# Performance work log

Measured on AMD Instinct MI355X. Metric: run time of the kernel, lower is better.

The kernel has to match this reference:

```python
import jax, jax.numpy as jnp
import numpy as np

SEQ, IN_DIM, OUT_DIM = 8192, 1024, 1024

def setup_inputs() -> dict:
    key = jax.random.key(0)
    k1, k2, k3, k4 = jax.random.split(key, 4)
    inputs = jax.random.normal(k1, (SEQ, IN_DIM), dtype=jnp.float32)
    # torch.nn.Linear stores weight as [out_dim, in_dim]; y = x @ W.T
    w_query = jax.random.normal(k2, (OUT_DIM, IN_DIM), dtype=jnp.float32) * (1.0 / np.sqrt(IN_DIM))
    w_key = jax.random.normal(k3, (OUT_DIM, IN_DIM), dtype=jnp.float32) * (1.0 / np.sqrt(IN_DIM))
    w_value = jax.random.normal(k4, (OUT_DIM, IN_DIM), dtype=jnp.float32) * (1.0 / np.sqrt(IN_DIM))
    return {"inputs": inputs, "w_query": w_query, "w_key": w_key, "w_value": w_value}

def reference(inputs, w_query, w_key, w_value):
    # QKV projections: [S, D_out]
    q = inputs @ w_query.T
    k = inputs @ w_key.T
    v = inputs @ w_value.T
    scale = 1.0 / jnp.sqrt(jnp.asarray(k.shape[-1], dtype=q.dtype))
    scores = (q @ k.T) * scale  # [S, S]
    # causal mask: lower-triangular kept, upper set to -inf
    s = scores.shape[0]
    causal = jnp.tril(jnp.ones((s, s), dtype=bool))
    scores = jnp.where(causal, scores, -jnp.inf)
    attn = jax.nn.softmax(scores, axis=-1)
    return attn @ v
```

## Files before the change

kernel.cpp:

```cpp
#include <hip/hip_runtime.h>
#include <stdint.h>
#include <stddef.h>


#define SEQ   8192
#define DIM   1024

typedef __bf16 bf16x8 __attribute__((ext_vector_type(8)));
typedef float  f32x4  __attribute__((ext_vector_type(4)));

#define MFMA16(a, b, c) __builtin_amdgcn_mfma_f32_16x16x32_bf16((a), (b), (c), 0, 0, 0)

__device__ __forceinline__ uint16_t f2bf(float f) {
  uint32_t u = __builtin_bit_cast(uint32_t, f);
  return (uint16_t)((u + 0x7fffu + ((u >> 16) & 1u)) >> 16);
}
__device__ __forceinline__ float bf2f(uint16_t h) {
  uint32_t u = ((uint32_t)h) << 16;
  return __builtin_bit_cast(float, u);
}

typedef const __attribute__((address_space(1))) uint32_t* gas_t;
typedef __attribute__((address_space(3))) uint32_t* las_t;
__device__ __forceinline__ void async16(const void* g, void* l) {
  __builtin_amdgcn_global_load_lds((gas_t)g, (las_t)l, 16, 0, 0);
}

__global__ __launch_bounds__(256) void cast_all(const float* __restrict__ x,
                                                const float* __restrict__ wq,
                                                const float* __restrict__ wk,
                                                const float* __restrict__ wv,
                                                uint16_t* __restrict__ xb,
                                                uint16_t* __restrict__ wcat) {
  int b = blockIdx.x;
  const float* src;
  uint16_t* dst;
  int i;
  if (b < 8192) {
    src = x; dst = xb; i = (b * 256 + threadIdx.x) * 4;
  } else {
    int wb = b - 8192;
    int sel = wb >> 10;
    src = sel == 0 ? wq : (sel == 1 ? wk : wv);
    dst = wcat + sel * 1048576;
    i = ((wb & 1023) * 256 + threadIdx.x) * 4;
  }
  float4 v = *(const float4*)(src + i);
  ushort4 o;
  o.x = f2bf(v.x); o.y = f2bf(v.y); o.z = f2bf(v.z); o.w = f2bf(v.w);
  *(ushort4*)(dst + i) = o;
}

__global__ __launch_bounds__(256) void qkv_gemm(const uint16_t* __restrict__ A,
                                                const uint16_t* __restrict__ B,
                                                uint16_t* __restrict__ Qblk,
                                                uint16_t* __restrict__ Kblk,
                                                uint16_t* __restrict__ Vblk) {
  __shared__ __align__(16) uint16_t Sh[16384];
  uint16_t* As = Sh;
  uint16_t* Bs = Sh + 8192;
  const int t    = threadIdx.x;
  const int w    = t >> 6;
  const int lane = t & 63;
  const int lm   = lane & 15;
  const int qd   = lane >> 4;
  const int wrow = (w >> 1) * 64;
  const int wcol = (w & 1) * 64;
  const int rowbase = blockIdx.y * 128;
  const int colbase = blockIdx.x * 128;

  const int lrow = lane >> 3;
  const int lgrp = (lane & 7) ^ (lrow & 7);

  f32x4 acc[4][4] = {};

  for (int kb = 0; kb < DIM; kb += 64) {
    __syncthreads();
#pragma unroll
    for (int rep = 0; rep < 4; ++rep) {
      int r0 = rep * 32 + w * 8;
      async16(A + (size_t)(rowbase + r0 + lrow) * DIM + kb + lgrp * 8, As + r0 * 64);
      async16(B + (size_t)(colbase + r0 + lrow) * DIM + kb + lgrp * 8, Bs + r0 * 64);
    }
    __syncthreads();
#pragma unroll
    for (int kc = 0; kc < 2; ++kc) {
      bf16x8 af[4], bfr[4];
#pragma unroll
      for (int mt = 0; mt < 4; ++mt) {
        int r = wrow + mt * 16 + lm;
        af[mt] = *(const bf16x8*)(As + r * 64 + (((kc * 4 + qd) ^ (lm & 7)) * 8));
      }
#pragma unroll
      for (int nt = 0; nt < 4; ++nt) {
        int r = wcol + nt * 16 + lm;
        bfr[nt] = *(const bf16x8*)(Bs + r * 64 + (((kc * 4 + qd) ^ (lm & 7)) * 8));
      }
#pragma unroll
      for (int mt = 0; mt < 4; ++mt)
#pragma unroll
        for (int nt = 0; nt < 4; ++nt)
          acc[mt][nt] = MFMA16(af[mt], bfr[nt], acc[mt][nt]);
    }
  }

  __syncthreads();
#pragma unroll
  for (int mt = 0; mt < 4; ++mt)
#pragma unroll
    for (int nt = 0; nt < 4; ++nt)
#pragma unroll
      for (int r = 0; r < 4; ++r) {
        int ml = wrow + mt * 16 + qd * 4 + r;
        int nl = wcol + nt * 16 + lm;
        uint16_t v = f2bf(acc[mt][nt][r]);
        int off;
        if (colbase < 2048) {
          off = ((ml >> 4) * 4 + (nl >> 5)) * 512 + ((nl >> 3) & 3) * 128 +
                (ml & 15) * 8 + (nl & 7);
        } else {
          off = ((nl >> 4) * 4 + (ml >> 5)) * 512 + ((ml >> 3) & 3) * 128 +
                (nl & 15) * 8 + (ml & 7);
        }
        Sh[off] = v;
      }
  __syncthreads();

  {
    uint16_t* dst = colbase < 1024 ? Qblk : (colbase < 2048 ? Kblk : Vblk);
    const int cb = colbase & 1023;
#pragma unroll
    for (int i = 0; i < 8; ++i) {
      int ch  = i * 256 + t;
      int tf  = ch >> 6;
      int idx = ch & 63;
      size_t gbase;
      if (colbase < 2048)
        gbase = ((size_t)((rowbase >> 4) + (tf >> 2)) * 32 + (cb >> 5) + (tf & 3)) * 512;
      else
        gbase = ((size_t)((cb >> 4) + (tf >> 2)) * 256 + (rowbase >> 5) + (tf & 3)) * 512;
      *(float4*)(dst + gbase + idx * 8) = *(const float4*)(Sh + tf * 512 + idx * 8);
    }
  }
}

__global__ __launch_bounds__(1024) void attn_kernel(const uint16_t* __restrict__ Qblk,
                                                    const uint16_t* __restrict__ Kblk,
                                                    const uint16_t* __restrict__ Vblk,
                                                    uint16_t* __restrict__ P0,
                                                    uint16_t* __restrict__ P1,
                                                    float* __restrict__ Mm,
                                                    float* __restrict__ Ll) {
  __shared__ __align__(16) uint16_t Qs[32768];
  __shared__ __align__(16) uint16_t Pb[8192];
  __shared__ float stats[32][16];
  __shared__ float mrow[32];

  const int t    = threadIdx.x;
  const int w    = t >> 6;
  const int lane = t & 63;
  const int lm   = lane & 15;
  const int qd   = lane >> 4;
  const int slot = blockIdx.x >> 3;
  const int p    = (blockIdx.x & 7) * 16 + (slot >> 1);
  const int par  = slot & 1;
  const float c1 = 0.045084220027780106f;

#pragma unroll 1
  for (int half = 0; half < 2; ++half) {
    const int tt   = half ? 255 - p : p;
    const int row0 = tt * 32;
    const int jn   = (tt >> 3) + 1;

    __syncthreads();
#pragma unroll
    for (int i = 0; i < 4; ++i)
      async16(Qblk + ((size_t)(tt * 64 + w * 4 + i)) * 512 + lane * 8,
              Qs + (w * 4 + i) * 512);

    bf16x8 kr[4];
    {
      const uint16_t* kbp0 = Kblk + ((size_t)(par * 16 + w) * 32) * 512 + lane * 8;
#pragma unroll
      for (int c = 0; c < 4; ++c)
        kr[c] = *(const bf16x8*)(kbp0 + (size_t)c * 512);
    }
    __syncthreads();

    float m_run[2][4], l_run[2][4];
#pragma unroll
    for (int mt = 0; mt < 2; ++mt)
#pragma unroll
      for (int r = 0; r < 4; ++r) { m_run[mt][r] = -1e30f; l_run[mt][r] = 0.0f; }
    f32x4 o_acc[2][4] = {};

#pragma unroll 1
    for (int jg = par; jg < jn; jg += 2) {
      const uint16_t* kbp = Kblk + ((size_t)(jg * 16 + w) * 32) * 512 + lane * 8;
      const uint16_t* vbp = Vblk + ((size_t)(w * 4) * 256 + jg * 8) * 512 + lane * 8;
      const uint16_t* qsp = Qs + lane * 8;

      f32x4 sacc[2] = {};
#pragma unroll
      for (int kb = 0; kb < 32; ++kb) {
        bf16x8 q0 = *(const bf16x8*)(qsp + kb * 512);
        bf16x8 q1 = *(const bf16x8*)(qsp + (32 + kb) * 512);
        bf16x8 kcur = kr[kb & 3];
        if (kb < 28)
          kr[kb & 3] = *(const bf16x8*)(kbp + (size_t)(kb + 4) * 512);
        sacc[0] = MFMA16(q0, kcur, sacc[0]);
        sacc[1] = MFMA16(q1, kcur, sacc[1]);
      }

      if (jg == jn - 1) {
#pragma unroll
        for (int mt = 0; mt < 2; ++mt)
#pragma unroll
          for (int r = 0; r < 4; ++r) {
            int col = jg * 256 + w * 16 + lm;
            int row = row0 + mt * 16 + qd * 4 + r;
            if (col > row) sacc[mt][r] = -1e30f;
          }
      }

#pragma unroll
      for (int mt = 0; mt < 2; ++mt)
#pragma unroll
        for (int r = 0; r < 4; ++r) {
          float v = sacc[mt][r];
          v = fmaxf(v, __shfl_xor(v, 1));
          v = fmaxf(v, __shfl_xor(v, 2));
          v = fmaxf(v, __shfl_xor(v, 4));
          v = fmaxf(v, __shfl_xor(v, 8));
          if (lm == 0) stats[mt * 16 + qd * 4 + r][w] = v;
        }
      __syncthreads();

      bf16x8 vr0[4], vr1[4];
#pragma unroll
      for (int dt = 0; dt < 4; ++dt)
        vr0[dt] = *(const bf16x8*)(vbp + ((size_t)dt * 256 + 0) * 512);

      float alpha[2][4], psum[2][4];
#pragma unroll
      for (int mt = 0; mt < 2; ++mt)
#pragma unroll
        for (int r = 0; r < 4; ++r) {
          int rl = mt * 16 + qd * 4 + r;
          float4 g0 = *(const float4*)&stats[rl][0];
          float4 g1 = *(const float4*)&stats[rl][4];
          float4 g2 = *(const float4*)&stats[rl][8];
          float4 g3 = *(const float4*)&stats[rl][12];
          float gm = fmaxf(
              fmaxf(fmaxf(fmaxf(g0.x, g0.y), fmaxf(g0.z, g0.w)),
                    fmaxf(fmaxf(g1.x, g1.y), fmaxf(g1.z, g1.w))),
              fmaxf(fmaxf(fmaxf(g2.x, g2.y), fmaxf(g2.z, g2.w)),
                    fmaxf(fmaxf(g3.x, g3.y), fmaxf(g3.z, g3.w))));
          float mn = fmaxf(m_run[mt][r], gm);
          alpha[mt][r] = exp2f((m_run[mt][r] - mn) * c1);
          m_run[mt][r] = mn;
          psum[mt][r] = 0.0f;
        }
#pragma unroll
      for (int mt = 0; mt < 2; ++mt)
#pragma unroll
        for (int r = 0; r < 4; ++r) {
          float pv = exp2f((sacc[mt][r] - m_run[mt][r]) * c1);
          psum[mt][r] += pv;
          Pb[((mt * 8 + (w >> 1)) * 64 + ((w & 1) * 2 + (lm >> 3)) * 16 +
              qd * 4 + r) * 8 + (lm & 7)] = f2bf(pv);
        }

#pragma unroll
      for (int dt = 0; dt < 4; ++dt)
        vr1[dt] = *(const bf16x8*)(vbp + ((size_t)dt * 256 + 1) * 512);

#pragma unroll
      for (int mt = 0; mt < 2; ++mt)
#pragma unroll
        for (int r = 0; r < 4; ++r) {
          float s2 = psum[mt][r];
          s2 += __shfl_xor(s2, 1);
          s2 += __shfl_xor(s2, 2);
          s2 += __shfl_xor(s2, 4);
          s2 += __shfl_xor(s2, 8);
          l_run[mt][r] = l_run[mt][r] * alpha[mt][r] + s2;
        }
      __syncthreads();

      {
        const uint16_t* kbpn = Kblk + ((size_t)((jg + 2) * 16 + w) * 32) * 512 + lane * 8;
#pragma unroll
        for (int c = 0; c < 4; ++c)
          kr[c] = *(const bf16x8*)(kbpn + (size_t)c * 512);
      }

#pragma unroll
      for (int mt = 0; mt < 2; ++mt)
#pragma unroll
        for (int dt = 0; dt < 4; ++dt)
#pragma unroll
          for (int r = 0; r < 4; ++r)
            o_acc[mt][dt][r] *= alpha[mt][r];

#pragma unroll
      for (int kc = 0; kc < 8; ++kc) {
        bf16x8 pf0 = *(const bf16x8*)(Pb + (kc * 64 + lane) * 8);
        bf16x8 pf1 = *(const bf16x8*)(Pb + ((8 + kc) * 64 + lane) * 8);
#pragma unroll
        for (int dt = 0; dt < 4; ++dt) {
          bf16x8 vf = (kc & 1) ? vr1[dt] : vr0[dt];
          o_acc[0][dt] = MFMA16(pf0, vf, o_acc[0][dt]);
          o_acc[1][dt] = MFMA16(pf1, vf, o_acc[1][dt]);
        }
        if (kc < 6) {
#pragma unroll
          for (int dt = 0; dt < 4; ++dt) {
            if (kc & 1)
              vr1[dt] = *(const bf16x8*)(vbp + ((size_t)dt * 256 + kc + 2) * 512);
            else
              vr0[dt] = *(const bf16x8*)(vbp + ((size_t)dt * 256 + kc + 2) * 512);
          }
        }
      }
    }

    if (lm == 0) {
#pragma unroll
      for (int mt = 0; mt < 2; ++mt)
#pragma unroll
        for (int r = 0; r < 4; ++r) {
          int rl = mt * 16 + qd * 4 + r;
          stats[rl][w] = l_run[mt][r];
          if (w == 0) mrow[rl] = m_run[mt][r];
        }
    }
    __syncthreads();
    if (t < 32) {
      float4 a0 = *(const float4*)&stats[t][0];
      float4 a1 = *(const float4*)&stats[t][4];
      float4 a2 = *(const float4*)&stats[t][8];
      float4 a3 = *(const float4*)&stats[t][12];
      Mm[par * SEQ + row0 + t] = mrow[t];
      Ll[par * SEQ + row0 + t] = (a0.x + a0.y + a0.z + a0.w) +
                                 (a1.x + a1.y + a1.z + a1.w) +
                                 (a2.x + a2.y + a2.z + a2.w) +
                                 (a3.x + a3.y + a3.z + a3.w);
    }
    uint16_t* Pp = par ? P1 : P0;
#pragma unroll
    for (int mt = 0; mt < 2; ++mt)
#pragma unroll
      for (int dt = 0; dt < 4; ++dt)
#pragma unroll
        for (int r = 0; r < 4; ++r) {
          int row = row0 + mt * 16 + qd * 4 + r;
          int d   = w * 64 + dt * 16 + lm;
          Pp[(size_t)row * DIM + d] = f2bf(o_acc[mt][dt][r]);
        }
  }
}

__global__ __launch_bounds__(256) void merge_kernel(const uint16_t* __restrict__ P0,
                                                    const uint16_t* __restrict__ P1,
                                                    const float* __restrict__ Mm,
                                                    const float* __restrict__ Ll,
                                                    float* __restrict__ out) {
  const int row = blockIdx.x;
  const int d0  = threadIdx.x * 4;
  const float c1 = 0.045084220027780106f;
  float m0 = Mm[row], m1 = Mm[SEQ + row];
  float l0 = Ll[row], l1 = Ll[SEQ + row];
  float m  = fmaxf(m0, m1);
  float a0 = exp2f((m0 - m) * c1);
  float a1 = exp2f((m1 - m) * c1);
  float inv = 1.0f / (a0 * l0 + a1 * l1);
  ushort4 p0 = *(const ushort4*)(P0 + (size_t)row * DIM + d0);
  ushort4 p1 = *(const ushort4*)(P1 + (size_t)row * DIM + d0);
  float4 o;
  o.x = (a0 * bf2f(p0.x) + a1 * bf2f(p1.x)) * inv;
  o.y = (a0 * bf2f(p0.y) + a1 * bf2f(p1.y)) * inv;
  o.z = (a0 * bf2f(p0.z) + a1 * bf2f(p1.z)) * inv;
  o.w = (a0 * bf2f(p0.w) + a1 * bf2f(p1.w)) * inv;
  *(float4*)(out + (size_t)row * DIM + d0) = o;
}

extern "C" void kernel_launch(void* const* d_in, const int* in_sizes, int n_in,
                              void* d_out, int out_size, void* d_ws, size_t ws_size,
                              hipStream_t stream) {
  (void)in_sizes; (void)n_in; (void)out_size; (void)ws_size;
  const float* x  = (const float*)d_in[0];
  const float* wq = (const float*)d_in[1];
  const float* wk = (const float*)d_in[2];
  const float* wv = (const float*)d_in[3];
  float* out = (float*)d_out;

  char* ws = (char*)d_ws;
  uint16_t* Qblk = (uint16_t*)(ws);
  uint16_t* Kblk = (uint16_t*)(ws + 16777216);
  uint16_t* Vblk = (uint16_t*)(ws + 33554432);
  uint16_t* P0   = (uint16_t*)(ws + 50331648);
  uint16_t* xb   = (uint16_t*)(ws + 67108864);
  uint16_t* P1   = (uint16_t*)(ws + 67108864);
  uint16_t* wcat = (uint16_t*)(ws + 83886080);
  float*    Mm   = (float*)(ws + 83886080);
  float*    Ll   = (float*)(ws + 83886080 + 65536);

  cast_all<<<11264, 256, 0, stream>>>(x, wq, wk, wv, xb, wcat);
  qkv_gemm<<<dim3(24, 64), 256, 0, stream>>>(xb, wcat, Qblk, Kblk, Vblk);
  attn_kernel<<<256, 1024, 0, stream>>>(Qblk, Kblk, Vblk, P0, P1, Mm, Ll);
  merge_kernel<<<SEQ, 256, 0, stream>>>(P0, P1, Mm, Ll, out);
}
```

Baseline: 494.9 us.

## Double-buffer QKV GEMM loads and fuse split-KV merge into attention via atomic flags

The QKV GEMM now double-buffers its LDS tiles, issuing async global-to-LDS loads for the next k-block while computing on the current one, with one barrier per iteration. The separate merge kernel is removed. Each attention block now increments a per-tile atomic counter after writing its partial output, and the second finisher combines both halves with the stored max and sum statistics and writes the final fp32 output. This saves a kernel launch and re-reading one partial, at the cost of doubled GEMM LDS (lower occupancy) and a fence plus atomic in the attention kernel.

```diff
diff --git a/kernel.cpp b/kernel.cpp
--- a/kernel.cpp
+++ b/kernel.cpp
@@ -5,6 +5,7 @@
 
 #define SEQ   8192
 #define DIM   1024
+#define MB    (1024 * 1024)
 
 typedef __bf16 bf16x8 __attribute__((ext_vector_type(8)));
 typedef float  f32x4  __attribute__((ext_vector_type(4)));
@@ -31,8 +32,10 @@
                                                 const float* __restrict__ wk,
                                                 const float* __restrict__ wv,
                                                 uint16_t* __restrict__ xb,
-                                                uint16_t* __restrict__ wcat) {
+                                                uint16_t* __restrict__ wcat,
+                                                int* __restrict__ Fl) {
   int b = blockIdx.x;
+  if (b == 0) Fl[threadIdx.x] = 0;
   const float* src;
   uint16_t* dst;
   int i;
@@ -56,9 +59,7 @@
                                                 uint16_t* __restrict__ Qblk,
                                                 uint16_t* __restrict__ Kblk,
                                                 uint16_t* __restrict__ Vblk) {
-  __shared__ __align__(16) uint16_t Sh[16384];
-  uint16_t* As = Sh;
-  uint16_t* Bs = Sh + 8192;
+  __shared__ __align__(16) uint16_t Sh[32768];
   const int t    = threadIdx.x;
   const int w    = t >> 6;
   const int lane = t & 63;
@@ -74,15 +75,30 @@
 
   f32x4 acc[4][4] = {};
 
-  for (int kb = 0; kb < DIM; kb += 64) {
-    __syncthreads();
-#pragma unroll
-    for (int rep = 0; rep < 4; ++rep) {
-      int r0 = rep * 32 + w * 8;
-      async16(A + (size_t)(rowbase + r0 + lrow) * DIM + kb + lgrp * 8, As + r0 * 64);
-      async16(B + (size_t)(colbase + r0 + lrow) * DIM + kb + lgrp * 8, Bs + r0 * 64);
-    }
-    __syncthreads();
+#pragma unroll
+  for (int rep = 0; rep < 4; ++rep) {
+    int r0 = rep * 32 + w * 8;
+    async16(A + (size_t)(rowbase + r0 + lrow) * DIM + lgrp * 8, Sh + r0 * 64);
+    async16(B + (size_t)(colbase + r0 + lrow) * DIM + lgrp * 8, Sh + 16384 + r0 * 64);
+  }
+  __syncthreads();
+
+  int cur = 0;
+  for (int it = 0; it < 16; ++it) {
+    if (it < 15) {
+      int kb = (it + 1) * 64;
+      int nxt = cur ^ 1;
+#pragma unroll
+      for (int rep = 0; rep < 4; ++rep) {
+        int r0 = rep * 32 + w * 8;
+        async16(A + (size_t)(rowbase + r0 + lrow) * DIM + kb + lgrp * 8,
+                Sh + nxt * 8192 + r0 * 64);
+        async16(B + (size_t)(colbase + r0 + lrow) * DIM + kb + lgrp * 8,
+                Sh + 16384 + nxt * 8192 + r0 * 64);
+      }
+    }
+    const uint16_t* As = Sh + cur * 8192;
+    const uint16_t* Bs = Sh + 16384 + cur * 8192;
 #pragma unroll
     for (int kc = 0; kc < 2; ++kc) {
       bf16x8 af[4], bfr[4];
@@ -102,9 +118,10 @@
         for (int nt = 0; nt < 4; ++nt)
           acc[mt][nt] = MFMA16(af[mt], bfr[nt], acc[mt][nt]);
     }
+    __syncthreads();
+    cur ^= 1;
   }
 
-  __syncthreads();
 #pragma unroll
   for (int mt = 0; mt < 4; ++mt)
 #pragma unroll
@@ -150,11 +167,16 @@
                                                     uint16_t* __restrict__ P0,
                                                     uint16_t* __restrict__ P1,
                                                     float* __restrict__ Mm,
-                                                    float* __restrict__ Ll) {
+                                                    float* __restrict__ Ll,
+                                                    int* __restrict__ Fl,
+                                                    float* __restrict__ out) {
   __shared__ __align__(16) uint16_t Qs[32768];
   __shared__ __align__(16) uint16_t Pb[8192];
   __shared__ float stats[32][16];
   __shared__ float mrow[32];
+  __shared__ float lrow[32];
+  __shared__ float coefS[32], coefO[32];
+  __shared__ int   flagSh;
 
   const int t    = threadIdx.x;
   const int w    = t >> 6;
@@ -341,11 +363,11 @@
       float4 a1 = *(const float4*)&stats[t][4];
       float4 a2 = *(const float4*)&stats[t][8];
       float4 a3 = *(const float4*)&stats[t][12];
+      float lsum = (a0.x + a0.y + a0.z + a0.w) + (a1.x + a1.y + a1.z + a1.w) +
+                   (a2.x + a2.y + a2.z + a2.w) + (a3.x + a3.y + a3.z + a3.w);
       Mm[par * SEQ + row0 + t] = mrow[t];
-      Ll[par * SEQ + row0 + t] = (a0.x + a0.y + a0.z + a0.w) +
-                                 (a1.x + a1.y + a1.z + a1.w) +
-                                 (a2.x + a2.y + a2.z + a2.w) +
-                                 (a3.x + a3.y + a3.z + a3.w);
+      Ll[par * SEQ + row0 + t] = lsum;
+      lrow[t] = lsum;
     }
     uint16_t* Pp = par ? P1 : P0;
 #pragma unroll
@@ -358,31 +380,41 @@
           int d   = w * 64 + dt * 16 + lm;
           Pp[(size_t)row * DIM + d] = f2bf(o_acc[mt][dt][r]);
         }
+
+    __threadfence();
+    __syncthreads();
+    if (t == 0) flagSh = atomicAdd(&Fl[tt], 1);
+    __syncthreads();
+    if (flagSh == 1) {
+      __threadfence();
+      if (t < 32) {
+        float m_o = Mm[(1 - par) * SEQ + row0 + t];
+        float l_o = Ll[(1 - par) * SEQ + row0 + t];
+        float m_s = mrow[t], l_s = lrow[t];
+        float mx  = fmaxf(m_s, m_o);
+        float as  = exp2f((m_s - mx) * c1);
+        float ao  = exp2f((m_o - mx) * c1);
+        float inv = 1.0f / (as * l_s + ao * l_o);
+        coefS[t] = as * inv;
+        coefO[t] = ao * inv;
+      }
+      __syncthreads();
+      const uint16_t* Po = par ? P0 : P1;
+#pragma unroll
+      for (int mt = 0; mt < 2; ++mt)
+#pragma unroll
+        for (int dt = 0; dt < 4; ++dt)
+#pragma unroll
+          for (int r = 0; r < 4; ++r) {
+            int rl  = mt * 16 + qd * 4 + r;
+            int row = row0 + rl;
+            int d   = w * 64 + dt * 16 + lm;
+            out[(size_t)row * DIM + d] =
+                coefS[rl] * o_acc[mt][dt][r] +
+                coefO[rl] * bf2f(Po[(size_t)row * DIM + d]);
+          }
+    }
   }
-}
-
-__global__ __launch_bounds__(256) void merge_kernel(const uint16_t* __restrict__ P0,
-                                                    const uint16_t* __restrict__ P1,
-                                                    const float* __restrict__ Mm,
-                                                    const float* __restrict__ Ll,
-                                                    float* __restrict__ out) {
-  const int row = blockIdx.x;
-  const int d0  = threadIdx.x * 4;
-  const float c1 = 0.045084220027780106f;
-  float m0 = Mm[row], m1 = Mm[SEQ + row];
-  float l0 = Ll[row], l1 = Ll[SEQ + row];
-  float m  = fmaxf(m0, m1);
-  float a0 = exp2f((m0 - m) * c1);
-  float a1 = exp2f((m1 - m) * c1);
-  float inv = 1.0f / (a0 * l0 + a1 * l1);
-  ushort4 p0 = *(const ushort4*)(P0 + (size_t)row * DIM + d0);
-  ushort4 p1 = *(const ushort4*)(P1 + (size_t)row * DIM + d0);
-  float4 o;
-  o.x = (a0 * bf2f(p0.x) + a1 * bf2f(p1.x)) * inv;
-  o.y = (a0 * bf2f(p0.y) + a1 * bf2f(p1.y)) * inv;
-  o.z = (a0 * bf2f(p0.z) + a1 * bf2f(p1.z)) * inv;
-  o.w = (a0 * bf2f(p0.w) + a1 * bf2f(p1.w)) * inv;
-  *(float4*)(out + (size_t)row * DIM + d0) = o;
 }
 
 extern "C" void kernel_launch(void* const* d_in, const int* in_sizes, int n_in,
@@ -397,17 +429,17 @@
 
   char* ws = (char*)d_ws;
   uint16_t* Qblk = (uint16_t*)(ws);
-  uint16_t* Kblk = (uint16_t*)(ws + 16777216);
-  uint16_t* Vblk = (uint16_t*)(ws + 33554432);
-  uint16_t* P0   = (uint16_t*)(ws + 50331648);
-  uint16_t* xb   = (uint16_t*)(ws + 67108864);
-  uint16_t* P1   = (uint16_t*)(ws + 67108864);
-  uint16_t* wcat = (uint16_t*)(ws + 83886080);
-  float*    Mm   = (float*)(ws + 83886080);
-  float*    Ll   = (float*)(ws + 83886080 + 65536);
-
-  cast_all<<<11264, 256, 0, stream>>>(x, wq, wk, wv, xb, wcat);
+  uint16_t* Kblk = (uint16_t*)(ws + 16 * MB);
+  uint16_t* Vblk = (uint16_t*)(ws + 32 * MB);
+  uint16_t* P0   = (uint16_t*)(ws + 48 * MB);
+  uint16_t* xb   = (uint16_t*)(ws + 64 * MB);
+  uint16_t* P1   = (uint16_t*)(ws + 64 * MB);
+  uint16_t* wcat = (uint16_t*)(ws + 80 * MB);
+  float*    Mm   = (float*)(ws + 80 * MB);
+  float*    Ll   = (float*)(ws + 80 * MB + 65536);
+  int*      Fl   = (int*)(ws + 88 * MB);
+
+  cast_all<<<11264, 256, 0, stream>>>(x, wq, wk, wv, xb, wcat, Fl);
   qkv_gemm<<<dim3(24, 64), 256, 0, stream>>>(xb, wcat, Qblk, Kblk, Vblk);
-  attn_kernel<<<256, 1024, 0, stream>>>(Qblk, Kblk, Vblk, P0, P1, Mm, Ll);
-  merge_kernel<<<SEQ, 256, 0, stream>>>(P0, P1, Mm, Ll, out);
-}
+  attn_kernel<<<256, 1024, 0, stream>>>(Qblk, Kblk, Vblk, P0, P1, Mm, Ll, Fl, out);
+}
```

New measurement: 888.9 us. 1.8x slower.

## Double-buffer QKV GEMM shared-memory tiles and hint attention occupancy

Applied to the files above, without the earlier changes.

The QKV projection GEMM now uses two shared-memory stages, so the async loads for the next K-slice are issued before computing on the current slice, with one barrier per iteration instead of two. This is meant to hide global-load latency behind MFMA work. It doubles the GEMM's LDS footprint to 64KB, which may lower occupancy. The attention kernel also gets a min-blocks launch-bounds hint that could change its register allocation.

```diff
diff --git a/kernel.cpp b/kernel.cpp
--- a/kernel.cpp
+++ b/kernel.cpp
@@ -5,6 +5,7 @@
 
 #define SEQ   8192
 #define DIM   1024
+#define MB    (1024 * 1024)
 
 typedef __bf16 bf16x8 __attribute__((ext_vector_type(8)));
 typedef float  f32x4  __attribute__((ext_vector_type(4)));
@@ -56,9 +57,7 @@
                                                 uint16_t* __restrict__ Qblk,
                                                 uint16_t* __restrict__ Kblk,
                                                 uint16_t* __restrict__ Vblk) {
-  __shared__ __align__(16) uint16_t Sh[16384];
-  uint16_t* As = Sh;
-  uint16_t* Bs = Sh + 8192;
+  __shared__ __align__(16) uint16_t Sh[32768];
   const int t    = threadIdx.x;
   const int w    = t >> 6;
   const int lane = t & 63;
@@ -74,15 +73,30 @@
 
   f32x4 acc[4][4] = {};
 
-  for (int kb = 0; kb < DIM; kb += 64) {
-    __syncthreads();
-#pragma unroll
-    for (int rep = 0; rep < 4; ++rep) {
-      int r0 = rep * 32 + w * 8;
-      async16(A + (size_t)(rowbase + r0 + lrow) * DIM + kb + lgrp * 8, As + r0 * 64);
-      async16(B + (size_t)(colbase + r0 + lrow) * DIM + kb + lgrp * 8, Bs + r0 * 64);
-    }
-    __syncthreads();
+#pragma unroll
+  for (int rep = 0; rep < 4; ++rep) {
+    int r0 = rep * 32 + w * 8;
+    async16(A + (size_t)(rowbase + r0 + lrow) * DIM + lgrp * 8, Sh + r0 * 64);
+    async16(B + (size_t)(colbase + r0 + lrow) * DIM + lgrp * 8, Sh + 16384 + r0 * 64);
+  }
+  __syncthreads();
+
+  int cur = 0;
+  for (int it = 0; it < 16; ++it) {
+    if (it < 15) {
+      int kb = (it + 1) * 64;
+      int nxt = cur ^ 1;
+#pragma unroll
+      for (int rep = 0; rep < 4; ++rep) {
+        int r0 = rep * 32 + w * 8;
+        async16(A + (size_t)(rowbase + r0 + lrow) * DIM + kb + lgrp * 8,
+                Sh + nxt * 8192 + r0 * 64);
+        async16(B + (size_t)(colbase + r0 + lrow) * DIM + kb + lgrp * 8,
+                Sh + 16384 + nxt * 8192 + r0 * 64);
+      }
+    }
+    const uint16_t* As = Sh + cur * 8192;
+    const uint16_t* Bs = Sh + 16384 + cur * 8192;
 #pragma unroll
     for (int kc = 0; kc < 2; ++kc) {
       bf16x8 af[4], bfr[4];
@@ -102,9 +116,10 @@
         for (int nt = 0; nt < 4; ++nt)
           acc[mt][nt] = MFMA16(af[mt], bfr[nt], acc[mt][nt]);
     }
+    __syncthreads();
+    cur ^= 1;
   }
 
-  __syncthreads();
 #pragma unroll
   for (int mt = 0; mt < 4; ++mt)
 #pragma unroll
@@ -144,13 +159,13 @@
   }
 }
 
-__global__ __launch_bounds__(1024) void attn_kernel(const uint16_t* __restrict__ Qblk,
-                                                    const uint16_t* __restrict__ Kblk,
-                                                    const uint16_t* __restrict__ Vblk,
-                                                    uint16_t* __restrict__ P0,
-                                                    uint16_t* __restrict__ P1,
-                                                    float* __restrict__ Mm,
-                                                    float* __restrict__ Ll) {
+__global__ __launch_bounds__(1024, 4) void attn_kernel(const uint16_t* __restrict__ Qblk,
+                                                       const uint16_t* __restrict__ Kblk,
+                                                       const uint16_t* __restrict__ Vblk,
+                                                       uint16_t* __restrict__ P0,
+                                                       uint16_t* __restrict__ P1,
+                                                       float* __restrict__ Mm,
+                                                       float* __restrict__ Ll) {
   __shared__ __align__(16) uint16_t Qs[32768];
   __shared__ __align__(16) uint16_t Pb[8192];
   __shared__ float stats[32][16];
@@ -397,14 +412,14 @@
 
   char* ws = (char*)d_ws;
   uint16_t* Qblk = (uint16_t*)(ws);
-  uint16_t* Kblk = (uint16_t*)(ws + 16777216);
-  uint16_t* Vblk = (uint16_t*)(ws + 33554432);
-  uint16_t* P0   = (uint16_t*)(ws + 50331648);
-  uint16_t* xb   = (uint16_t*)(ws + 67108864);
-  uint16_t* P1   = (uint16_t*)(ws + 67108864);
-  uint16_t* wcat = (uint16_t*)(ws + 83886080);
-  float*    Mm   = (float*)(ws + 83886080);
-  float*    Ll   = (float*)(ws + 83886080 + 65536);
+  uint16_t* Kblk = (uint16_t*)(ws + 16 * MB);
+  uint16_t* Vblk = (uint16_t*)(ws + 32 * MB);
+  uint16_t* P0   = (uint16_t*)(ws + 48 * MB);
+  uint16_t* xb   = (uint16_t*)(ws + 64 * MB);
+  uint16_t* P1   = (uint16_t*)(ws + 64 * MB);
+  uint16_t* wcat = (uint16_t*)(ws + 80 * MB);
+  float*    Mm   = (float*)(ws + 80 * MB);
+  float*    Ll   = (float*)(ws + 80 * MB + 65536);
 
   cast_all<<<11264, 256, 0, stream>>>(x, wq, wk, wv, xb, wcat);
   qkv_gemm<<<dim3(24, 64), 256, 0, stream>>>(xb, wcat, Qblk, Kblk, Vblk);
```

Result: slower. 513.6 us (+3.8%).
